# Kernel tuning notes

Hardware: AMD Instinct MI355X
Metric: run time of the kernel (lower is better)

## Reference

```python
import jax, jax.numpy as jnp
import numpy as np

B_SZ = 8
D_MODEL = 512
D_STATE = 64
N2 = D_STATE // 2  # S4D uses complex-conjugate pairs -> d_state//2 complex modes
L_SEQ = 2048


def setup_inputs() -> dict:
    key = jax.random.key(0)
    ks = jax.random.split(key, 16)
    d = D_MODEL
    scale = 1.0 / np.sqrt(d)
    inp = {
        "x": jax.random.normal(ks[0], (B_SZ, d, L_SEQ), dtype=jnp.float32),
        # q/k/v projections (nn.Linear: weight (out,in), bias (out,))
        "Wq": jax.random.normal(ks[1], (d, d), dtype=jnp.float32) * scale,
        "bq": jax.random.normal(ks[2], (d,), dtype=jnp.float32) * scale,
        "Wk": jax.random.normal(ks[3], (d, d), dtype=jnp.float32) * scale,
        "bk": jax.random.normal(ks[4], (d,), dtype=jnp.float32) * scale,
        "Wv": jax.random.normal(ks[5], (d, d), dtype=jnp.float32) * scale,
        "bv": jax.random.normal(ks[6], (d,), dtype=jnp.float32) * scale,
        # Shift layer params
        "shift_C": jax.random.normal(ks[7], (1, d, D_STATE), dtype=jnp.float32),
        "shift_D": jax.random.normal(ks[8], (d,), dtype=jnp.float32),
        # S4D (diagonal SSM) params
        "log_dt": jax.random.uniform(ks[9], (d,), dtype=jnp.float32,
                                      minval=np.log(1e-3), maxval=np.log(1e-1)),
        "A_real": jnp.log(0.5 * jnp.ones((d, N2), dtype=jnp.float32)),
        "A_imag": jnp.broadcast_to(np.pi * jnp.arange(N2, dtype=jnp.float32), (d, N2)),
        "C_re": jax.random.normal(ks[10], (d, N2), dtype=jnp.float32) * np.sqrt(0.5),
        "C_im": jax.random.normal(ks[11], (d, N2), dtype=jnp.float32) * np.sqrt(0.5),
        "s4_D": jax.random.normal(ks[12], (d,), dtype=jnp.float32),
    }
    return inp


def _linear_chan(x, W, b):
    # x: (B, H, L); Linear applied over channel dim H -> (B, H_out, L)
    return jnp.einsum("bhl,dh->bdl", x, W) + b[:, None]


def _shift(u, C, Dp):
    """Shift SSM: causal conv with kernel = first L taps of C (computed via FFT
    exactly as the torch source does). u: (B, H, L)."""
    L = u.shape[-1]
    n = 2 * L
    H, S = C.shape[1], C.shape[2]
    Bmat = jnp.zeros((H, S), dtype=u.dtype).at[:, 0].set(1.0)
    B_fc = jnp.conj(jnp.fft.rfft(Bmat, n=n, axis=-1))  # (H, L+1)
    C_f = jnp.fft.rfft(C, n=n, axis=-1)                # (1, H, L+1)
    kernel = jnp.fft.irfft(B_fc * C_f, n=n, axis=-1)[..., :L]  # (1, H, L)
    kernel_f = jnp.fft.rfft(kernel, n=n, axis=-1)      # (1, H, L+1)
    u_f = jnp.fft.rfft(u, n=n, axis=-1)                # (B, H, L+1)
    y = jnp.fft.irfft(u_f * kernel_f, n=n, axis=-1)[..., :L]
    return y + u * Dp[:, None]


def _s4d(u, log_dt, A_real, A_imag, C_re, C_im, Dp):
    """Standard S4D forward: ZOH-discretized diagonal SSM kernel + FFT conv.
    u: (B, H, L)."""
    L = u.shape[-1]
    n = 2 * L
    dt = jnp.exp(log_dt)[:, None]                  # (H, 1)
    A = -jnp.exp(A_real) + 1j * A_imag             # (H, N2)
    dtA = A * dt                                   # (H, N2)
    C = (C_re + 1j * C_im) * (jnp.exp(dtA) - 1.0) / A
    vand = jnp.exp(dtA[:, :, None] * jnp.arange(L))  # (H, N2, L)
    K = 2.0 * jnp.einsum("hn,hnl->hl", C, vand).real  # (H, L)
    y = jnp.fft.irfft(jnp.fft.rfft(u, n=n, axis=-1) * jnp.fft.rfft(K, n=n, axis=-1),
                      n=n, axis=-1)[..., :L]
    return y + u * Dp[:, None]


def reference(x, Wq, bq, Wk, bk, Wv, bv, shift_C, shift_D,
              log_dt, A_real, A_imag, C_re, C_im, s4_D):
    q = _linear_chan(x, Wq, bq)
    k = _linear_chan(x, Wk, bk)
    v = _linear_chan(x, Wv, bv)
    shift_out = _shift(k, shift_C, shift_D)
    s4d_out = _s4d(v * shift_out, log_dt, A_real, A_imag, C_re, C_im, s4_D)
    return q * s4d_out
```

## Files before the change

kernel.cpp:

```cpp
#include <hip/hip_runtime.h>
#include <cstdint>


#define DMODEL 512
#define LSEQ 2048

typedef _Float16 half_t;
typedef __attribute__((ext_vector_type(2))) _Float16 half2v;
typedef __attribute__((ext_vector_type(4))) _Float16 half4v;
typedef __attribute__((ext_vector_type(8))) _Float16 half8v;
typedef __attribute__((ext_vector_type(4))) float floatx4;

#define SW(R, c) ((R) * 64 + ((((c) >> 3) ^ ((R) & 7)) << 3) + ((c) & 7))

__device__ __forceinline__ void gload_lds16(const half_t* g, half_t* l) {
  __builtin_amdgcn_global_load_lds(
      (const __attribute__((address_space(1))) uint32_t*)g,
      (__attribute__((address_space(3))) uint32_t*)l, 16, 0, 0);
}

#define WAIT_LGKM_BAR()                                   \
  do {                                                    \
    asm volatile("s_waitcnt lgkmcnt(0)" ::: "memory");    \
    __builtin_amdgcn_s_barrier();                         \
    __builtin_amdgcn_sched_barrier(0);                    \
  } while (0)

__global__ __launch_bounds__(256) void prep(
    const float* __restrict__ x, const float* __restrict__ Wq,
    const float* __restrict__ Wk, const float* __restrict__ Wv,
    half_t* __restrict__ xT, half_t* __restrict__ W16) {
  __shared__ float tile[64][68];
  int bid = blockIdx.x;
  int tid = threadIdx.x;
  if (bid < 2048) {
    int b = bid >> 8, rem = bid & 255;
    int d0 = (rem >> 5) * 64, l0 = (rem & 31) * 64;
    int dy = tid >> 4, lx = tid & 15;
    const float* xp = x + ((size_t)(b * 512 + d0)) * 2048 + l0;
#pragma unroll
    for (int rr = 0; rr < 4; rr++) {
      float4 v = *(const float4*)(xp + (size_t)(rr * 16 + dy) * 2048 + lx * 4);
      *(float4*)&tile[rr * 16 + dy][lx * 4] = v;
    }
    __syncthreads();
    half_t* op = xT + ((size_t)(b * 2048 + l0)) * 512 + d0;
    int lr = tid >> 2, c4 = tid & 3;
#pragma unroll
    for (int cc = 0; cc < 2; cc++) {
      int ch = cc * 4 + c4;
      half8v hv;
#pragma unroll
      for (int e = 0; e < 8; e++) hv[e] = (half_t)tile[ch * 8 + e][lr];
      *(half8v*)(op + (size_t)lr * 512 + ch * 8) = hv;
    }
  } else {
    int base = (bid - 2048) * 256 + tid;
#pragma unroll
    for (int it = 0; it < 6; it++) {
      int i = base + it * 131072;
      const float* src = (i < 262144) ? Wq : ((i < 524288) ? Wk : Wv);
      W16[i] = (half_t)src[i & 262143];
    }
  }
}

__global__ __launch_bounds__(256) void gemm_qkv(
    const half_t* __restrict__ xT, const half_t* __restrict__ Wstk,
    const float* __restrict__ bq, const float* __restrict__ bk,
    const float* __restrict__ bv, half_t* __restrict__ outq,
    half_t* __restrict__ outk, half_t* __restrict__ outv) {
  __shared__ half_t smem[16384];
  half_t* As = smem;
  half_t* Bs = smem + 8192;
  int flat = blockIdx.x;
  int swz = (flat & 7) * 192 + (flat >> 3);
  int nt = swz / 12, mt = swz - nt * 12;
  int n0 = nt * 128, m0 = mt * 128;
  int tid = threadIdx.x;
  int lane = tid & 63, wid = tid >> 6;
  int wr = wid >> 1, wc = wid & 1;
  int lrow = lane & 15, lg = lane >> 4;
  int rsub = lane >> 3, ssub = lane & 7;
  int gslot = ssub ^ rsub;

  floatx4 acc[4][4];
#pragma unroll
  for (int i = 0; i < 4; i++)
#pragma unroll
    for (int j = 0; j < 4; j++) acc[i][j] = (floatx4){0.f, 0.f, 0.f, 0.f};

  const half_t* gA = Wstk + (size_t)(m0 + wid * 32 + rsub) * 512 + gslot * 8;
  const half_t* gB = xT + (size_t)(n0 + wid * 32 + rsub) * 512 + gslot * 8;

  for (int kk = 0; kk < 512; kk += 64) {
#pragma unroll
    for (int i = 0; i < 4; i++) {
      int c = wid * 4 + i;
      gload_lds16(gA + (size_t)i * 8 * 512 + kk, As + c * 512);
      gload_lds16(gB + (size_t)i * 8 * 512 + kk, Bs + c * 512);
    }
    __syncthreads();
#pragma unroll
    for (int h = 0; h < 2; h++) {
      half8v af[4], bf[4];
#pragma unroll
      for (int i = 0; i < 4; i++) {
        int r = wr * 64 + i * 16 + lrow;
        af[i] = *(const half8v*)(As + r * 64 + ((h * 4 + lg) ^ (r & 7)) * 8);
      }
#pragma unroll
      for (int j = 0; j < 4; j++) {
        int r = wc * 64 + j * 16 + lrow;
        bf[j] = *(const half8v*)(Bs + r * 64 + ((h * 4 + lg) ^ (r & 7)) * 8);
      }
#pragma unroll
      for (int i = 0; i < 4; i++)
#pragma unroll
        for (int j = 0; j < 4; j++)
          acc[i][j] = __builtin_amdgcn_mfma_f32_16x16x32_f16(af[i], bf[j],
                                                             acc[i][j], 0, 0, 0);
    }
    __syncthreads();
  }

  int z = m0 >> 9;
  const float* bias = (z == 0) ? bq : ((z == 1) ? bk : bv);
  half_t* smemC = smem;
#pragma unroll
  for (int i = 0; i < 4; i++) {
    int dl = wr * 64 + i * 16 + 4 * lg;
    float4 b4 = *(const float4*)&bias[(m0 + dl) & 511];
#pragma unroll
    for (int j = 0; j < 4; j++) {
      int ll = wc * 64 + j * 16 + lrow;
#pragma unroll
      for (int reg = 0; reg < 4; reg++) {
        int d = dl + reg;
        float val = acc[i][j][reg] + ((const float*)&b4)[reg];
        smemC[d * 128 + (((ll >> 3) ^ (d & 15)) << 3) + (ll & 7)] = (half_t)val;
      }
    }
  }
  __syncthreads();
  {
    int t4 = tid >> 4, ch = tid & 15;
    int b = n0 >> 11, l0 = n0 & 2047;
    half_t* outp = (z == 0) ? outq : ((z == 1) ? outk : outv);
#pragma unroll
    for (int rep = 0; rep < 8; rep++) {
      int d = rep * 16 + t4;
      half8v v = *(const half8v*)(smemC + d * 128 + ((ch ^ (d & 15)) << 3));
      size_t rowb = ((size_t)(b * 512 + ((m0 + d) & 511))) * 2048;
      if (z == 0) {
        *(half8v*)(outp + rowb + l0 + ch * 8) = v;
      } else {
        int j = (l0 >> 6) + (ch >> 3);
        int s = ch & 7;
        *(half8v*)(outp + rowb + j * 64 + ((s ^ (j & 7)) << 3)) = v;
      }
    }
  }
}

__global__ __launch_bounds__(256) void s4d_main(
    const half_t* __restrict__ kimg, const half_t* __restrict__ vimg,
    const float* __restrict__ shC, const float* __restrict__ log_dt,
    const float* __restrict__ A_real, const float* __restrict__ A_imag,
    const float* __restrict__ C_re, const float* __restrict__ C_im,
    const float* __restrict__ shD, const float* __restrict__ s4D,
    const half_t* __restrict__ qbuf, float* __restrict__ outp) {
  __shared__ half_t tabs[5][4096];
  __shared__ half_t kl[2][33 * 64];
  __shared__ half_t vg[2][32 * 64];
  __shared__ half_t uh[32 * 64];
  __shared__ float SG[32 * 66];
  int h = blockIdx.x;
  int tid = threadIdx.x;
  int lane = tid & 63, wid = tid >> 6;
  int lrow = lane & 15, lg = lane >> 4;
  int mi = wid & 1, ri0 = wid >> 1;

  gload_lds16(kimg + (size_t)h * 2048 + wid * 512 + lane * 8,
              &kl[0][64 + wid * 512]);
  gload_lds16(vimg + (size_t)h * 2048 + wid * 512 + lane * 8,
              &vg[0][wid * 512]);
  if (tid < 16) {
    half8v zz = {(_Float16)0, (_Float16)0, (_Float16)0, (_Float16)0,
                 (_Float16)0, (_Float16)0, (_Float16)0, (_Float16)0};
    *(half8v*)(&kl[tid >> 3][(tid & 7) * 8]) = zz;
  }

  float* Kt   = SG;
  float* tapl = SG + 64;
  float* aL   = SG + 128;
  float* bL   = SG + 160;
  float* wrL  = SG + 192;
  float* wiL  = SG + 224;
  float* crL  = SG + 256;
  float* ciL  = SG + 288;
  if (tid < 64) { Kt[tid] = 0.f; tapl[tid] = shC[h * 64 + tid]; }
  if (tid < 32) {
    int n = tid, hn = h * 32 + n;
    float dt = expf(log_dt[h]);
    float Ar = -expf(A_real[hn]), Ai = A_imag[hn];
    float a = dt * Ar, b = dt * Ai;
    float ea = expf(a);
    float wr = ea * cosf(b), wi = ea * sinf(b);
    float Am2 = Ar * Ar + Ai * Ai;
    float zr = wr - 1.0f, zi = wi;
    float qr = (zr * Ar + zi * Ai) / Am2;
    float qi = (zi * Ar - zr * Ai) / Am2;
    aL[n] = a; bL[n] = b; wrL[n] = wr; wiL[n] = wi;
    crL[n] = C_re[hn] * qr - C_im[hn] * qi;
    ciL[n] = C_re[hn] * qi + C_im[hn] * qr;
  }
  __syncthreads();
  float wTr, wTi;
  {
    int n = tid & 31;
    float e64 = expf(64.f * aL[n]);
    float b64 = 64.f * bL[n];
    wTr = e64 * cosf(b64);
    wTi = e64 * sinf(b64);
  }
  {
    int r = tid >> 2, nb = (tid & 3) * 8;
    float ksum = 0.f;
#pragma unroll
    for (int i = 0; i < 8; i++) {
      int n = nb + i;
      float a = aL[n], b = bL[n];
      float cr = crL[n], ci = ciL[n];
      float er = expf(a * (float)r);
      float w0r = er * cosf(b * (float)r), w0i = er * sinf(b * (float)r);
      ksum += 2.f * (cr * w0r - ci * w0i);
      float wr = wrL[n], wi = wiL[n];
      float w1r = w0r * wr - w0i * wi, w1i = w0r * wi + w0i * wr;
      tabs[3][SW(r, 2 * n)]     = (half_t)(2.f * (cr * w1r - ci * w1i));
      tabs[3][SW(r, 2 * n + 1)] = (half_t)(-2.f * (cr * w1i + ci * w1r));
      tabs[2][SW(2 * n, 63 - r)]     = (half_t)w0r;
      tabs[2][SW(2 * n + 1, 63 - r)] = (half_t)w0i;
    }
    atomicAdd(&Kt[r], ksum);
  }
  __syncthreads();
#pragma unroll
  for (int e = 0; e < 16; e++) {
    int idx = e * 256 + tid;
    int r = idx >> 6, t = idx & 63;
    int d = r - t;
    int a = SW(r, t);
    tabs[4][a] = (d >= 0) ? (half_t)Kt[d] : (half_t)0.f;
    tabs[0][a] = (d >= 0) ? (half_t)tapl[d] : (half_t)0.f;
    tabs[1][a] = (d < 0) ? (half_t)tapl[64 + d] : (half_t)0.f;
  }
  float sDsh = shD[h];
  float sD4 = s4D[h];
  const half_t* t1 = tabs[0];
  const half_t* t2 = tabs[1];
  const half_t* tV = tabs[2];
  const half_t* tE = tabs[3];
  const half_t* tT = tabs[4];

#define LDF(base, r, ks, key) \
  (*(const half8v*)((base) + (r) * 64 + (((ks) * 4 + lg) ^ (key)) * 8))

  int cur = 0;
  for (int bi = 0; bi < 8; bi++) {
    if (bi < 7) {
      size_t nb = (size_t)((bi + 1) * 512 + h) * 2048;
      gload_lds16(kimg + nb + wid * 512 + lane * 8, &kl[cur ^ 1][64 + wid * 512]);
      gload_lds16(vimg + nb + wid * 512 + lane * 8, &vg[cur ^ 1][wid * 512]);
      asm volatile("s_waitcnt vmcnt(2) lgkmcnt(0)" ::: "memory");
    } else {
      asm volatile("s_waitcnt vmcnt(0) lgkmcnt(0)" ::: "memory");
    }
    __builtin_amdgcn_s_barrier();
    __builtin_amdgcn_sched_barrier(0);

    const half_t* klc = kl[cur];
    half_t* vgc = vg[cur];
    floatx4 acc[2];

    acc[0] = (floatx4){0.f, 0.f, 0.f, 0.f};
    acc[1] = (floatx4){0.f, 0.f, 0.f, 0.f};
    {
      int jA = mi * 16 + lrow;
      int key1 = lrow & 7, key2 = (lrow + 7) & 7;
#pragma unroll
      for (int ks = 0; ks < 2; ks++) {
        half8v a1 = LDF(klc, 1 + jA, ks, key1);
        half8v a2 = LDF(klc, jA, ks, key2);
#pragma unroll
        for (int tt = 0; tt < 2; tt++) {
          int rb = (ri0 + tt * 2) * 16 + lrow;
          half8v b1 = LDF(t1, rb, ks, lrow & 7);
          half8v b2 = LDF(t2, rb, ks, lrow & 7);
          acc[tt] = __builtin_amdgcn_mfma_f32_16x16x32_f16(a1, b1, acc[tt], 0, 0, 0);
          acc[tt] = __builtin_amdgcn_mfma_f32_16x16x32_f16(a2, b2, acc[tt], 0, 0, 0);
        }
      }
    }
#pragma unroll
    for (int tt = 0; tt < 2; tt++) {
#pragma unroll
      for (int reg = 0; reg < 4; reg++) {
        int j = mi * 16 + 4 * lg + reg;
        int r = (ri0 + tt * 2) * 16 + lrow;
        int cph = (((r >> 3) ^ (j & 7)) << 3) + (r & 7);
        float kvv = (float)klc[(1 + j) * 64 + cph];
        float vvv = (float)vgc[j * 64 + cph];
        uh[j * 64 + cph] = (half_t)(vvv * (acc[tt][reg] + sDsh * kvv));
      }
    }
    WAIT_LGKM_BAR();

    acc[0] = (floatx4){0.f, 0.f, 0.f, 0.f};
    acc[1] = (floatx4){0.f, 0.f, 0.f, 0.f};
#pragma unroll
    for (int ks = 0; ks < 2; ks++) {
      half8v a = LDF(uh, mi * 16 + lrow, ks, lrow & 7);
#pragma unroll
      for (int tt = 0; tt < 2; tt++) {
        int rb = (ri0 + tt * 2) * 16 + lrow;
        half8v b = LDF(tV, rb, ks, lrow & 7);
        acc[tt] = __builtin_amdgcn_mfma_f32_16x16x32_f16(a, b, acc[tt], 0, 0, 0);
      }
    }
#pragma unroll
    for (int tt = 0; tt < 2; tt++) {
      int ri = ri0 + tt * 2;
#pragma unroll
      for (int reg = 0; reg < 4; reg++) {
        int j = mi * 16 + 4 * lg + reg;
        SG[j * 66 + ri * 16 + lrow] = acc[tt][reg];
      }
    }
    WAIT_LGKM_BAR();

    if (tid < 32) {
      int n = tid;
      float gr = 0.f, gi = 0.f;
#pragma unroll 4
      for (int j = 0; j < 32; j++) {
        float tr = SG[j * 66 + 2 * n], ti = SG[j * 66 + 2 * n + 1];
        half2v gp = {(half_t)gr, (half_t)gi};
        *(half2v*)(vgc + j * 64 + (((n >> 2) ^ (j & 7)) << 3) + 2 * (n & 3)) = gp;
        float nr = wTr * gr - wTi * gi + tr;
        gi = wTr * gi + wTi * gr + ti;
        gr = nr;
      }
    }
    WAIT_LGKM_BAR();

    acc[0] = (floatx4){0.f, 0.f, 0.f, 0.f};
    acc[1] = (floatx4){0.f, 0.f, 0.f, 0.f};
#pragma unroll
    for (int ks = 0; ks < 2; ks++) {
      half8v ag = LDF(vgc, mi * 16 + lrow, ks, lrow & 7);
      half8v au = LDF(uh, mi * 16 + lrow, ks, lrow & 7);
#pragma unroll
      for (int tt = 0; tt < 2; tt++) {
        int rb = (ri0 + tt * 2) * 16 + lrow;
        half8v be = LDF(tE, rb, ks, lrow & 7);
        half8v bt = LDF(tT, rb, ks, lrow & 7);
        acc[tt] = __builtin_amdgcn_mfma_f32_16x16x32_f16(ag, be, acc[tt], 0, 0, 0);
        acc[tt] = __builtin_amdgcn_mfma_f32_16x16x32_f16(au, bt, acc[tt], 0, 0, 0);
      }
    }
#pragma unroll
    for (int tt = 0; tt < 2; tt++) {
#pragma unroll
      for (int reg = 0; reg < 4; reg++) {
        int j = mi * 16 + 4 * lg + reg;
        int r = (ri0 + tt * 2) * 16 + lrow;
        int cph = (((r >> 3) ^ (j & 7)) << 3) + (r & 7);
        SG[j * 64 + r] = acc[tt][reg] + sD4 * (float)uh[j * 64 + cph];
      }
    }
    WAIT_LGKM_BAR();

    {
      size_t bh = (size_t)(bi * 512 + h) * 2048;
      half8v qv = *(const half8v*)(qbuf + bh + tid * 8);
      float* op = outp + bh;
      float4 o0, o1;
      o0.x = (float)qv[0] * SG[tid * 8 + 0];
      o0.y = (float)qv[1] * SG[tid * 8 + 1];
      o0.z = (float)qv[2] * SG[tid * 8 + 2];
      o0.w = (float)qv[3] * SG[tid * 8 + 3];
      o1.x = (float)qv[4] * SG[tid * 8 + 4];
      o1.y = (float)qv[5] * SG[tid * 8 + 5];
      o1.z = (float)qv[6] * SG[tid * 8 + 6];
      o1.w = (float)qv[7] * SG[tid * 8 + 7];
      *(float4*)(op + tid * 8) = o0;
      *(float4*)(op + tid * 8 + 4) = o1;
    }
    cur ^= 1;
  }
#undef LDF
}

extern "C" void kernel_launch(void* const* d_in, const int* in_sizes, int n_in,
                              void* d_out, int out_size, void* d_ws, size_t ws_size,
                              hipStream_t stream) {
  const float* x      = (const float*)d_in[0];
  const float* Wq     = (const float*)d_in[1];
  const float* bq     = (const float*)d_in[2];
  const float* Wk     = (const float*)d_in[3];
  const float* bk     = (const float*)d_in[4];
  const float* Wv     = (const float*)d_in[5];
  const float* bv     = (const float*)d_in[6];
  const float* shC    = (const float*)d_in[7];
  const float* shD    = (const float*)d_in[8];
  const float* log_dt = (const float*)d_in[9];
  const float* A_real = (const float*)d_in[10];
  const float* A_imag = (const float*)d_in[11];
  const float* C_re   = (const float*)d_in[12];
  const float* C_im   = (const float*)d_in[13];
  const float* s4D    = (const float*)d_in[14];
  float* out = (float*)d_out;
  half_t* wsh = (half_t*)d_ws;

  half_t* qbuf = wsh;
  half_t* kbuf = wsh + 8388608;
  half_t* vbuf = wsh + 16777216;
  half_t* xT16 = wsh + 25165824;
  half_t* W16  = wsh + 33554432;

  prep<<<2560, 256, 0, stream>>>(x, Wq, Wk, Wv, xT16, W16);
  gemm_qkv<<<dim3(1536), 256, 0, stream>>>(xT16, W16, bq, bk, bv,
                                           qbuf, kbuf, vbuf);
  s4d_main<<<512, 256, 0, stream>>>(kbuf, vbuf, shC, log_dt, A_real, A_imag,
                                    C_re, C_im, shD, s4D, qbuf, out);
}
```

Before: 84.75 us.

## Launch one block per (batch, channel) instead of looping batches per channel

The s4d_main kernel previously ran 512 blocks, each looping over 8 batches with double-buffered k/v loads. It now launches 4096 blocks, one per batch-channel pair, removing the batch loop and double buffering. Table buffers are time-shared: the shift tables are overwritten with the S4D tables after the first stage, which cuts LDS use and raises occupancy. The price is that every block recomputes the per-channel SSM tables (exp/sin/cos), eight times more of that setup work overall.

```diff
diff --git a/kernel.cpp b/kernel.cpp
--- a/kernel.cpp
+++ b/kernel.cpp
@@ -170,35 +170,40 @@
     const float* __restrict__ C_re, const float* __restrict__ C_im,
     const float* __restrict__ shD, const float* __restrict__ s4D,
     const half_t* __restrict__ qbuf, float* __restrict__ outp) {
-  __shared__ half_t tabs[5][4096];
-  __shared__ half_t kl[2][33 * 64];
-  __shared__ half_t vg[2][32 * 64];
+  __shared__ half_t kl[33 * 64];
+  __shared__ half_t vg[32 * 64];
   __shared__ half_t uh[32 * 64];
+  __shared__ half_t tabA[4096];
+  __shared__ half_t tabB[4096];
+  __shared__ half_t tabC[4096];
   __shared__ float SG[32 * 66];
-  int h = blockIdx.x;
+  __shared__ float scr[384];
+  int bh = blockIdx.x;
+  int h = bh & 511;
   int tid = threadIdx.x;
   int lane = tid & 63, wid = tid >> 6;
   int lrow = lane & 15, lg = lane >> 4;
   int mi = wid & 1, ri0 = wid >> 1;
 
-  gload_lds16(kimg + (size_t)h * 2048 + wid * 512 + lane * 8,
-              &kl[0][64 + wid * 512]);
-  gload_lds16(vimg + (size_t)h * 2048 + wid * 512 + lane * 8,
-              &vg[0][wid * 512]);
-  if (tid < 16) {
+  float* Kt   = scr;
+  float* tapl = scr + 64;
+  float* aL   = scr + 128;
+  float* bL   = scr + 160;
+  float* wrL  = scr + 192;
+  float* wiL  = scr + 224;
+  float* crL  = scr + 256;
+  float* ciL  = scr + 288;
+  float* wTL  = scr + 320;
+
+  gload_lds16(kimg + (size_t)bh * 2048 + wid * 512 + lane * 8,
+              kl + 64 + wid * 512);
+  gload_lds16(vimg + (size_t)bh * 2048 + wid * 512 + lane * 8,
+              vg + wid * 512);
+  if (tid < 8) {
     half8v zz = {(_Float16)0, (_Float16)0, (_Float16)0, (_Float16)0,
                  (_Float16)0, (_Float16)0, (_Float16)0, (_Float16)0};
-    *(half8v*)(&kl[tid >> 3][(tid & 7) * 8]) = zz;
-  }
-
-  float* Kt   = SG;
-  float* tapl = SG + 64;
-  float* aL   = SG + 128;
-  float* bL   = SG + 160;
-  float* wrL  = SG + 192;
-  float* wiL  = SG + 224;
-  float* crL  = SG + 256;
-  float* ciL  = SG + 288;
+    *(half8v*)(kl + tid * 8) = zz;
+  }
   if (tid < 64) { Kt[tid] = 0.f; tapl[tid] = shC[h * 64 + tid]; }
   if (tid < 32) {
     int n = tid, hn = h * 32 + n;
@@ -214,16 +219,13 @@
     aL[n] = a; bL[n] = b; wrL[n] = wr; wiL[n] = wi;
     crL[n] = C_re[hn] * qr - C_im[hn] * qi;
     ciL[n] = C_re[hn] * qi + C_im[hn] * qr;
+    float e64 = expf(64.f * a);
+    wTL[2 * n]     = e64 * cosf(64.f * b);
+    wTL[2 * n + 1] = e64 * sinf(64.f * b);
   }
   __syncthreads();
-  float wTr, wTi;
-  {
-    int n = tid & 31;
-    float e64 = expf(64.f * aL[n]);
-    float b64 = 64.f * bL[n];
-    wTr = e64 * cosf(b64);
-    wTi = e64 * sinf(b64);
-  }
+
+  half_t eR[8], eI[8];
   {
     int r = tid >> 2, nb = (tid & 3) * 8;
     float ksum = 0.f;
@@ -237,167 +239,162 @@
       ksum += 2.f * (cr * w0r - ci * w0i);
       float wr = wrL[n], wi = wiL[n];
       float w1r = w0r * wr - w0i * wi, w1i = w0r * wi + w0i * wr;
-      tabs[3][SW(r, 2 * n)]     = (half_t)(2.f * (cr * w1r - ci * w1i));
-      tabs[3][SW(r, 2 * n + 1)] = (half_t)(-2.f * (cr * w1i + ci * w1r));
-      tabs[2][SW(2 * n, 63 - r)]     = (half_t)w0r;
-      tabs[2][SW(2 * n + 1, 63 - r)] = (half_t)w0i;
+      eR[i] = (half_t)(2.f * (cr * w1r - ci * w1i));
+      eI[i] = (half_t)(-2.f * (cr * w1i + ci * w1r));
+      tabC[SW(2 * n, 63 - r)]     = (half_t)w0r;
+      tabC[SW(2 * n + 1, 63 - r)] = (half_t)w0i;
     }
     atomicAdd(&Kt[r], ksum);
   }
-  __syncthreads();
 #pragma unroll
   for (int e = 0; e < 16; e++) {
     int idx = e * 256 + tid;
     int r = idx >> 6, t = idx & 63;
     int d = r - t;
     int a = SW(r, t);
-    tabs[4][a] = (d >= 0) ? (half_t)Kt[d] : (half_t)0.f;
-    tabs[0][a] = (d >= 0) ? (half_t)tapl[d] : (half_t)0.f;
-    tabs[1][a] = (d < 0) ? (half_t)tapl[64 + d] : (half_t)0.f;
+    tabA[a] = (d >= 0) ? (half_t)tapl[d] : (half_t)0.f;
+    tabB[a] = (d < 0) ? (half_t)tapl[64 + d] : (half_t)0.f;
   }
   float sDsh = shD[h];
   float sD4 = s4D[h];
-  const half_t* t1 = tabs[0];
-  const half_t* t2 = tabs[1];
-  const half_t* tV = tabs[2];
-  const half_t* tE = tabs[3];
-  const half_t* tT = tabs[4];
+  float wTr = wTL[2 * (tid & 31)], wTi = wTL[2 * (tid & 31) + 1];
+  asm volatile("s_waitcnt vmcnt(0) lgkmcnt(0)" ::: "memory");
+  __builtin_amdgcn_s_barrier();
+  __builtin_amdgcn_sched_barrier(0);
 
 #define LDF(base, r, ks, key) \
   (*(const half8v*)((base) + (r) * 64 + (((ks) * 4 + lg) ^ (key)) * 8))
 
-  int cur = 0;
-  for (int bi = 0; bi < 8; bi++) {
-    if (bi < 7) {
-      size_t nb = (size_t)((bi + 1) * 512 + h) * 2048;
-      gload_lds16(kimg + nb + wid * 512 + lane * 8, &kl[cur ^ 1][64 + wid * 512]);
-      gload_lds16(vimg + nb + wid * 512 + lane * 8, &vg[cur ^ 1][wid * 512]);
-      asm volatile("s_waitcnt vmcnt(2) lgkmcnt(0)" ::: "memory");
-    } else {
-      asm volatile("s_waitcnt vmcnt(0) lgkmcnt(0)" ::: "memory");
-    }
-    __builtin_amdgcn_s_barrier();
-    __builtin_amdgcn_sched_barrier(0);
-
-    const half_t* klc = kl[cur];
-    half_t* vgc = vg[cur];
-    floatx4 acc[2];
-
-    acc[0] = (floatx4){0.f, 0.f, 0.f, 0.f};
-    acc[1] = (floatx4){0.f, 0.f, 0.f, 0.f};
-    {
-      int jA = mi * 16 + lrow;
-      int key1 = lrow & 7, key2 = (lrow + 7) & 7;
-#pragma unroll
-      for (int ks = 0; ks < 2; ks++) {
-        half8v a1 = LDF(klc, 1 + jA, ks, key1);
-        half8v a2 = LDF(klc, jA, ks, key2);
-#pragma unroll
-        for (int tt = 0; tt < 2; tt++) {
-          int rb = (ri0 + tt * 2) * 16 + lrow;
-          half8v b1 = LDF(t1, rb, ks, lrow & 7);
-          half8v b2 = LDF(t2, rb, ks, lrow & 7);
-          acc[tt] = __builtin_amdgcn_mfma_f32_16x16x32_f16(a1, b1, acc[tt], 0, 0, 0);
-          acc[tt] = __builtin_amdgcn_mfma_f32_16x16x32_f16(a2, b2, acc[tt], 0, 0, 0);
-        }
-      }
-    }
-#pragma unroll
-    for (int tt = 0; tt < 2; tt++) {
-#pragma unroll
-      for (int reg = 0; reg < 4; reg++) {
-        int j = mi * 16 + 4 * lg + reg;
-        int r = (ri0 + tt * 2) * 16 + lrow;
-        int cph = (((r >> 3) ^ (j & 7)) << 3) + (r & 7);
-        float kvv = (float)klc[(1 + j) * 64 + cph];
-        float vvv = (float)vgc[j * 64 + cph];
-        uh[j * 64 + cph] = (half_t)(vvv * (acc[tt][reg] + sDsh * kvv));
-      }
-    }
-    WAIT_LGKM_BAR();
-
-    acc[0] = (floatx4){0.f, 0.f, 0.f, 0.f};
-    acc[1] = (floatx4){0.f, 0.f, 0.f, 0.f};
+  floatx4 acc[2];
+  acc[0] = (floatx4){0.f, 0.f, 0.f, 0.f};
+  acc[1] = (floatx4){0.f, 0.f, 0.f, 0.f};
+  {
+    int jA = mi * 16 + lrow;
+    int key1 = lrow & 7, key2 = (lrow + 7) & 7;
 #pragma unroll
     for (int ks = 0; ks < 2; ks++) {
-      half8v a = LDF(uh, mi * 16 + lrow, ks, lrow & 7);
+      half8v a1 = LDF(kl, 1 + jA, ks, key1);
+      half8v a2 = LDF(kl, jA, ks, key2);
 #pragma unroll
       for (int tt = 0; tt < 2; tt++) {
         int rb = (ri0 + tt * 2) * 16 + lrow;
-        half8v b = LDF(tV, rb, ks, lrow & 7);
-        acc[tt] = __builtin_amdgcn_mfma_f32_16x16x32_f16(a, b, acc[tt], 0, 0, 0);
+        half8v b1 = LDF(tabA, rb, ks, lrow & 7);
+        half8v b2 = LDF(tabB, rb, ks, lrow & 7);
+        acc[tt] = __builtin_amdgcn_mfma_f32_16x16x32_f16(a1, b1, acc[tt], 0, 0, 0);
+        acc[tt] = __builtin_amdgcn_mfma_f32_16x16x32_f16(a2, b2, acc[tt], 0, 0, 0);
       }
     }
+  }
+#pragma unroll
+  for (int tt = 0; tt < 2; tt++) {
+#pragma unroll
+    for (int reg = 0; reg < 4; reg++) {
+      int j = mi * 16 + 4 * lg + reg;
+      int r = (ri0 + tt * 2) * 16 + lrow;
+      int cph = (((r >> 3) ^ (j & 7)) << 3) + (r & 7);
+      float kvv = (float)kl[(1 + j) * 64 + cph];
+      float vvv = (float)vg[j * 64 + cph];
+      uh[j * 64 + cph] = (half_t)(vvv * (acc[tt][reg] + sDsh * kvv));
+    }
+  }
+  WAIT_LGKM_BAR();
+
+  {
+    int r = tid >> 2, nb = (tid & 3) * 8;
+#pragma unroll
+    for (int i = 0; i < 8; i++) {
+      int n = nb + i;
+      tabA[SW(r, 2 * n)]     = eR[i];
+      tabA[SW(r, 2 * n + 1)] = eI[i];
+    }
+  }
+#pragma unroll
+  for (int e = 0; e < 16; e++) {
+    int idx = e * 256 + tid;
+    int r = idx >> 6, t = idx & 63;
+    int d = r - t;
+    tabB[SW(r, t)] = (d >= 0) ? (half_t)Kt[d] : (half_t)0.f;
+  }
+  acc[0] = (floatx4){0.f, 0.f, 0.f, 0.f};
+  acc[1] = (floatx4){0.f, 0.f, 0.f, 0.f};
+#pragma unroll
+  for (int ks = 0; ks < 2; ks++) {
+    half8v a = LDF(uh, mi * 16 + lrow, ks, lrow & 7);
 #pragma unroll
     for (int tt = 0; tt < 2; tt++) {
-      int ri = ri0 + tt * 2;
-#pragma unroll
-      for (int reg = 0; reg < 4; reg++) {
-        int j = mi * 16 + 4 * lg + reg;
-        SG[j * 66 + ri * 16 + lrow] = acc[tt][reg];
-      }
-    }
-    WAIT_LGKM_BAR();
-
-    if (tid < 32) {
-      int n = tid;
-      float gr = 0.f, gi = 0.f;
+      int rb = (ri0 + tt * 2) * 16 + lrow;
+      half8v b = LDF(tabC, rb, ks, lrow & 7);
+      acc[tt] = __builtin_amdgcn_mfma_f32_16x16x32_f16(a, b, acc[tt], 0, 0, 0);
+    }
+  }
+#pragma unroll
+  for (int tt = 0; tt < 2; tt++) {
+    int ri = ri0 + tt * 2;
+#pragma unroll
+    for (int reg = 0; reg < 4; reg++) {
+      int j = mi * 16 + 4 * lg + reg;
+      SG[j * 66 + ri * 16 + lrow] = acc[tt][reg];
+    }
+  }
+  WAIT_LGKM_BAR();
+
+  if (tid < 32) {
+    int n = tid;
+    float gr = 0.f, gi = 0.f;
 #pragma unroll 4
-      for (int j = 0; j < 32; j++) {
-        float tr = SG[j * 66 + 2 * n], ti = SG[j * 66 + 2 * n + 1];
-        half2v gp = {(half_t)gr, (half_t)gi};
-        *(half2v*)(vgc + j * 64 + (((n >> 2) ^ (j & 7)) << 3) + 2 * (n & 3)) = gp;
-        float nr = wTr * gr - wTi * gi + tr;
-        gi = wTr * gi + wTi * gr + ti;
-        gr = nr;
-      }
-    }
-    WAIT_LGKM_BAR();
-
-    acc[0] = (floatx4){0.f, 0.f, 0.f, 0.f};
-    acc[1] = (floatx4){0.f, 0.f, 0.f, 0.f};
-#pragma unroll
-    for (int ks = 0; ks < 2; ks++) {
-      half8v ag = LDF(vgc, mi * 16 + lrow, ks, lrow & 7);
-      half8v au = LDF(uh, mi * 16 + lrow, ks, lrow & 7);
-#pragma unroll
-      for (int tt = 0; tt < 2; tt++) {
-        int rb = (ri0 + tt * 2) * 16 + lrow;
-        half8v be = LDF(tE, rb, ks, lrow & 7);
-        half8v bt = LDF(tT, rb, ks, lrow & 7);
-        acc[tt] = __builtin_amdgcn_mfma_f32_16x16x32_f16(ag, be, acc[tt], 0, 0, 0);
-        acc[tt] = __builtin_amdgcn_mfma_f32_16x16x32_f16(au, bt, acc[tt], 0, 0, 0);
-      }
-    }
+    for (int j = 0; j < 32; j++) {
+      float tr = SG[j * 66 + 2 * n], ti = SG[j * 66 + 2 * n + 1];
+      half2v gp = {(half_t)gr, (half_t)gi};
+      *(half2v*)(vg + j * 64 + (((n >> 2) ^ (j & 7)) << 3) + 2 * (n & 3)) = gp;
+      float nr = wTr * gr - wTi * gi + tr;
+      gi = wTr * gi + wTi * gr + ti;
+      gr = nr;
+    }
+  }
+  WAIT_LGKM_BAR();
+
+  acc[0] = (floatx4){0.f, 0.f, 0.f, 0.f};
+  acc[1] = (floatx4){0.f, 0.f, 0.f, 0.f};
+#pragma unroll
+  for (int ks = 0; ks < 2; ks++) {
+    half8v ag = LDF(vg, mi * 16 + lrow, ks, lrow & 7);
+    half8v au = LDF(uh, mi * 16 + lrow, ks, lrow & 7);
 #pragma unroll
     for (int tt = 0; tt < 2; tt++) {
-#pragma unroll
-      for (int reg = 0; reg < 4; reg++) {
-        int j = mi * 16 + 4 * lg + reg;
-        int r = (ri0 + tt * 2) * 16 + lrow;
-        int cph = (((r >> 3) ^ (j & 7)) << 3) + (r & 7);
-        SG[j * 64 + r] = acc[tt][reg] + sD4 * (float)uh[j * 64 + cph];
-      }
-    }
-    WAIT_LGKM_BAR();
-
-    {
-      size_t bh = (size_t)(bi * 512 + h) * 2048;
-      half8v qv = *(const half8v*)(qbuf + bh + tid * 8);
-      float* op = outp + bh;
-      float4 o0, o1;
-      o0.x = (float)qv[0] * SG[tid * 8 + 0];
-      o0.y = (float)qv[1] * SG[tid * 8 + 1];
-      o0.z = (float)qv[2] * SG[tid * 8 + 2];
-      o0.w = (float)qv[3] * SG[tid * 8 + 3];
-      o1.x = (float)qv[4] * SG[tid * 8 + 4];
-      o1.y = (float)qv[5] * SG[tid * 8 + 5];
-      o1.z = (float)qv[6] * SG[tid * 8 + 6];
-      o1.w = (float)qv[7] * SG[tid * 8 + 7];
-      *(float4*)(op + tid * 8) = o0;
-      *(float4*)(op + tid * 8 + 4) = o1;
-    }
-    cur ^= 1;
+      int rb = (ri0 + tt * 2) * 16 + lrow;
+      half8v be = LDF(tabA, rb, ks, lrow & 7);
+      half8v bt = LDF(tabB, rb, ks, lrow & 7);
+      acc[tt] = __builtin_amdgcn_mfma_f32_16x16x32_f16(ag, be, acc[tt], 0, 0, 0);
+      acc[tt] = __builtin_amdgcn_mfma_f32_16x16x32_f16(au, bt, acc[tt], 0, 0, 0);
+    }
+  }
+#pragma unroll
+  for (int tt = 0; tt < 2; tt++) {
+#pragma unroll
+    for (int reg = 0; reg < 4; reg++) {
+      int j = mi * 16 + 4 * lg + reg;
+      int r = (ri0 + tt * 2) * 16 + lrow;
+      int cph = (((r >> 3) ^ (j & 7)) << 3) + (r & 7);
+      SG[j * 64 + r] = acc[tt][reg] + sD4 * (float)uh[j * 64 + cph];
+    }
+  }
+  WAIT_LGKM_BAR();
+
+  {
+    size_t base = (size_t)bh * 2048;
+    half8v qv = *(const half8v*)(qbuf + base + tid * 8);
+    float* op = outp + base;
+    float4 o0, o1;
+    o0.x = (float)qv[0] * SG[tid * 8 + 0];
+    o0.y = (float)qv[1] * SG[tid * 8 + 1];
+    o0.z = (float)qv[2] * SG[tid * 8 + 2];
+    o0.w = (float)qv[3] * SG[tid * 8 + 3];
+    o1.x = (float)qv[4] * SG[tid * 8 + 4];
+    o1.y = (float)qv[5] * SG[tid * 8 + 5];
+    o1.z = (float)qv[6] * SG[tid * 8 + 6];
+    o1.w = (float)qv[7] * SG[tid * 8 + 7];
+    *(float4*)(op + tid * 8) = o0;
+    *(float4*)(op + tid * 8 + 4) = o1;
   }
 #undef LDF
 }
@@ -432,6 +429,6 @@
   prep<<<2560, 256, 0, stream>>>(x, Wq, Wk, Wv, xT16, W16);
   gemm_qkv<<<dim3(1536), 256, 0, stream>>>(xT16, W16, bq, bk, bv,
                                            qbuf, kbuf, vbuf);
-  s4d_main<<<512, 256, 0, stream>>>(kbuf, vbuf, shC, log_dt, A_real, A_imag,
-                                    C_re, C_im, shD, s4D, qbuf, out);
+  s4d_main<<<4096, 256, 0, stream>>>(kbuf, vbuf, shC, log_dt, A_real, A_imag,
+                                     C_re, C_im, shD, s4D, qbuf, out);
 }
```

After: 114.8 us. 35.4% more time.
